# Optimization experiments

Hardware: AMD Instinct MI355X
Metric: run time of the kernel (lower is better)

## Reference

```python
import jax, jax.numpy as jnp
import numpy as np
from jax import lax

M, N, D = 4096, 4096, 256
SINKHORN_ITERATIONS = 100
SINKHORN_EPSILON = 0.1
DESC_SCALE = 0.05  # keep exp(S/eps) finite for random descriptors


def setup_inputs() -> dict:
    key = jax.random.key(0)
    k1, k2 = jax.random.split(key)
    d_M_q = jax.random.normal(k1, (M, D), dtype=jnp.float32) * DESC_SCALE
    d_N_r = jax.random.normal(k2, (N, D), dtype=jnp.float32) * DESC_SCALE
    z = jnp.float32(0.5)  # SuperGlue bin_score default
    return {"d_M_q": d_M_q, "d_N_r": d_N_r, "z": z}


def reference(d_M_q, d_N_r, z):
    m, n = d_M_q.shape[0], d_N_r.shape[0]
    # score matrix [M, N]
    S = jnp.einsum('md,nd->mn', d_M_q, d_N_r)
    # augment with dustbin row/col filled with z -> [M+1, N+1]
    dtype = d_M_q.dtype
    last_col = jnp.full((m, 1), z, dtype=dtype)
    last_row = jnp.full((1, n + 1), z, dtype=dtype)
    S_aug = jnp.concatenate([jnp.concatenate([S, last_col], axis=1), last_row], axis=0)
    K = jnp.exp(S_aug / SINKHORN_EPSILON)

    def step(K, _):
        K = K / K.sum(axis=1, keepdims=True)  # row normalize
        K = K / K.sum(axis=0, keepdims=True)  # col normalize
        return K, None

    K, _ = lax.scan(step, K, None, length=SINKHORN_ITERATIONS)
    P = K[:m, :n]
    return P, K
```

## Files before the change

### kernel.cpp

```cpp
#include <hip/hip_runtime.h>
#include <hip/hip_bf16.h>


#define MROWS 4096
#define NCOLS 4096
#define DDIM 256
#define MP1 4097
#define INV_EPS 10.0f
#define NBLK 256
#define XSLOT 4160
#define BAR_DW 160

typedef __attribute__((ext_vector_type(8))) short bf16x8;
typedef __attribute__((ext_vector_type(4))) float f32x4;
typedef __attribute__((ext_vector_type(2))) float f32x2;
typedef __attribute__((ext_vector_type(4))) unsigned short u16x4;

static __device__ __forceinline__ unsigned short f2bf(float f) {
  __hip_bfloat16 h = __float2bfloat16(f);
  union { __hip_bfloat16 h; unsigned short s; } c;
  c.h = h;
  return c.s;
}

static __device__ __forceinline__ void ld_strip(const float* ps, float4& xv) {
  asm volatile("global_load_dwordx4 %0, %1, off sc0\n\t"
               "s_waitcnt vmcnt(0)"
               : "=v"(xv) : "v"(ps) : "memory");
}
static __device__ __forceinline__ void ld_strip_dust(const float* ps, const float* pd,
                                                     float4& xv, float& xd) {
  asm volatile("global_load_dwordx4 %0, %2, off sc0\n\t"
               "global_load_dword %1, %3, off sc0\n\t"
               "s_waitcnt vmcnt(0)"
               : "=v"(xv), "=v"(xd)
               : "v"(ps), "v"(pd)
               : "memory");
}
static __device__ __forceinline__ void st_coherent(float* p, float x) {
  asm volatile("global_store_dword %0, %1, off sc0 sc1" :: "v"(p), "v"(x) : "memory");
}
static __device__ __forceinline__ unsigned ld_flagc(const unsigned* p) {
  unsigned r;
  asm volatile("global_load_dword %0, %1, off sc0 sc1\n\t"
               "s_waitcnt vmcnt(0)"
               : "=v"(r) : "v"(p) : "memory");
  return r;
}

template <int MODE>
__global__ __launch_bounds__(256) void mfma_gemm_kernel(
    const float* __restrict__ Q, const float* __restrict__ R,
    unsigned char* __restrict__ A8, unsigned char* __restrict__ T8,
    float* __restrict__ Kf, float* __restrict__ P,
    const float* __restrict__ u, const float* __restrict__ v)
{
  __shared__ unsigned short Qs[128][40];
  __shared__ unsigned short Rs[128][40];

  const int tid = threadIdx.x;
  const int lane = tid & 63;
  const int wid = tid >> 6;
  const int wy = wid >> 1;
  const int wx = wid & 1;
  const int rb = blockIdx.y * 128;
  const int cb = blockIdx.x * 128;
  const int lr = tid >> 3;
  const int lf = (tid & 7) * 4;

  f32x4 acc[4][4];
#pragma unroll
  for (int m = 0; m < 4; ++m)
#pragma unroll
    for (int n = 0; n < 4; ++n)
      acc[m][n] = (f32x4){0.f, 0.f, 0.f, 0.f};

  for (int k0 = 0; k0 < DDIM; k0 += 32) {
    float4 qv[4], rv[4];
#pragma unroll
    for (int i = 0; i < 4; ++i) {
      qv[i] = *reinterpret_cast<const float4*>(&Q[(size_t)(rb + lr + 32 * i) * DDIM + k0 + lf]);
      rv[i] = *reinterpret_cast<const float4*>(&R[(size_t)(cb + lr + 32 * i) * DDIM + k0 + lf]);
    }
    __syncthreads();
#pragma unroll
    for (int i = 0; i < 4; ++i) {
      u16x4 qs = {f2bf(qv[i].x), f2bf(qv[i].y), f2bf(qv[i].z), f2bf(qv[i].w)};
      u16x4 rs = {f2bf(rv[i].x), f2bf(rv[i].y), f2bf(rv[i].z), f2bf(rv[i].w)};
      *reinterpret_cast<u16x4*>(&Qs[lr + 32 * i][lf]) = qs;
      *reinterpret_cast<u16x4*>(&Rs[lr + 32 * i][lf]) = rs;
    }
    __syncthreads();

    const int ko = (lane >> 4) * 8;
    const int fr = lane & 15;
    bf16x8 af[4], bg[4];
#pragma unroll
    for (int m = 0; m < 4; ++m)
      af[m] = *reinterpret_cast<const bf16x8*>(&Qs[wy * 64 + m * 16 + fr][ko]);
#pragma unroll
    for (int n = 0; n < 4; ++n)
      bg[n] = *reinterpret_cast<const bf16x8*>(&Rs[wx * 64 + n * 16 + fr][ko]);
#pragma unroll
    for (int m = 0; m < 4; ++m)
#pragma unroll
      for (int n = 0; n < 4; ++n)
        acc[m][n] = __builtin_amdgcn_mfma_f32_16x16x32_bf16(af[m], bg[n], acc[m][n], 0, 0, 0);
  }

  const int r0 = (lane >> 4) * 4;
  const int fc = lane & 15;
#pragma unroll
  for (int m = 0; m < 4; ++m) {
    const int row0 = rb + wy * 64 + m * 16 + r0;
    float uu[4];
    if (MODE == 1) {
#pragma unroll
      for (int r = 0; r < 4; ++r) uu[r] = u[row0 + r];
    }
#pragma unroll
    for (int n = 0; n < 4; ++n) {
      const int col = cb + wx * 64 + n * 16 + fc;
      if (MODE == 0) {
        float kv[4];
#pragma unroll
        for (int r = 0; r < 4; ++r) kv[r] = __expf(acc[m][n][r] * INV_EPS);
        int packed = __builtin_amdgcn_cvt_pk_fp8_f32(kv[0], kv[1], 0, false);
        packed = __builtin_amdgcn_cvt_pk_fp8_f32(kv[2], kv[3], packed, true);
        *reinterpret_cast<unsigned int*>(&T8[(size_t)col * NCOLS + row0]) = (unsigned int)packed;
#pragma unroll
        for (int r = 0; r < 4; ++r)
          A8[(size_t)(row0 + r) * NCOLS + col] = (unsigned char)(((unsigned int)packed >> (8 * r)) & 0xffu);
      } else {
        const float vc = v[col];
#pragma unroll
        for (int r = 0; r < 4; ++r) {
          const float kv = __expf(acc[m][n][r] * INV_EPS);
          const float val = uu[r] * kv * vc;
          Kf[(size_t)(row0 + r) * MP1 + col] = val;
          P[(size_t)(row0 + r) * NCOLS + col] = val;
        }
      }
    }
  }
}

__global__ void init_sync_kernel(float* __restrict__ xbuf, unsigned* __restrict__ bar)
{
  const int i = blockIdx.x * 1024 + threadIdx.x;
  if (i < MP1) xbuf[i] = 1.0f;
  if (i < BAR_DW) bar[i] = 0u;
}

__global__ void edgeK_kernel(const float* __restrict__ zp, float* __restrict__ Kf,
                             const float* __restrict__ u, const float* __restrict__ v)
{
  const int i = blockIdx.x * 256 + threadIdx.x;
  if (i >= MP1) return;
  const float E = __expf(zp[0] * INV_EPS);
  Kf[(size_t)i * MP1 + NCOLS] = u[i] * E * v[NCOLS];
  Kf[(size_t)MROWS * MP1 + i] = u[MROWS] * E * v[i];
}

__global__ __launch_bounds__(1024) void sinkhorn_persist_kernel(
    const unsigned char* __restrict__ A8, const unsigned char* __restrict__ T8,
    float* __restrict__ xbuf, const float* __restrict__ zp,
    unsigned* __restrict__ bar)
{
  __shared__ unsigned char lA[16 * 4096];
  __shared__ unsigned char lT[16 * 4096];
  __shared__ float scratch[2][16][17];
  __shared__ float dscr[2][16];

  const int tid = threadIdx.x;
  const int b = blockIdx.x;
  const int lane = tid & 63;
  const int w = tid >> 6;
  const float E = __expf(zp[0] * INV_EPS);
  const int rev4 = ((lane & 1) << 3) | ((lane & 2) << 1) | ((lane & 4) >> 1) | ((lane & 8) >> 3);

  unsigned* cg  = bar + ((b & 7) << 4);
  unsigned* cm  = bar + 128;
  unsigned* gen = bar + 144;

  {
    const uint4* gA = reinterpret_cast<const uint4*>(A8 + (size_t)b * 16 * 4096);
    const uint4* gT = reinterpret_cast<const uint4*>(T8 + (size_t)b * 16 * 4096);
    uint4* sA = reinterpret_cast<uint4*>(lA);
    uint4* sT = reinterpret_cast<uint4*>(lT);
#pragma unroll
    for (int i = 0; i < 4; ++i) {
      sA[tid + 1024 * i] = gA[tid + 1024 * i];
      sT[tid + 1024 * i] = gT[tid + 1024 * i];
    }
  }
  __syncthreads();

  const int c0 = (w << 8) + (lane << 2);

  for (int g = 1; g <= 200; ++g) {
    const unsigned char* Kl = (g & 1) ? lA : lT;
    const float* xin = xbuf + (size_t)(g - 1) * XSLOT;
    float* xout = xbuf + (size_t)g * XSLOT;
    const unsigned need = (unsigned)(g - 1);
    const int sb = g & 1;

    if (tid == 0) {
      unsigned gv = ld_flagc(gen);
      while (gv < need) {
        __builtin_amdgcn_s_sleep(1);
        gv = ld_flagc(gen);
      }
    }
    __syncthreads();

    float4 xv; float xd = 0.f;
    if (w == 0) ld_strip_dust(xin + c0, xin + 4096, xv, xd);
    else        ld_strip(xin + c0, xv);

    float acc[16];
#pragma unroll
    for (int r = 0; r < 16; ++r) {
      const unsigned int aw = *reinterpret_cast<const unsigned int*>(Kl + r * 4096 + c0);
      const f32x2 lo = __builtin_amdgcn_cvt_pk_f32_fp8((int)aw, false);
      const f32x2 hi = __builtin_amdgcn_cvt_pk_f32_fp8((int)aw, true);
      acc[r] = lo.x * xv.x + lo.y * xv.y + hi.x * xv.z + hi.y * xv.w;
    }

    float r8[8], r4[4], r2[2], r1;
    {
      const bool f0 = (lane & 1) != 0;
#pragma unroll
      for (int k = 0; k < 8; ++k) {
        const float send = f0 ? acc[k] : acc[k + 8];
        const float keep = f0 ? acc[k + 8] : acc[k];
        r8[k] = keep + __shfl_xor(send, 1, 64);
      }
      const bool f1 = (lane & 2) != 0;
#pragma unroll
      for (int k = 0; k < 4; ++k) {
        const float send = f1 ? r8[k] : r8[k + 4];
        const float keep = f1 ? r8[k + 4] : r8[k];
        r4[k] = keep + __shfl_xor(send, 2, 64);
      }
      const bool f2 = (lane & 4) != 0;
#pragma unroll
      for (int k = 0; k < 2; ++k) {
        const float send = f2 ? r4[k] : r4[k + 2];
        const float keep = f2 ? r4[k + 2] : r4[k];
        r2[k] = keep + __shfl_xor(send, 4, 64);
      }
      const bool f3 = (lane & 8) != 0;
      {
        const float send = f3 ? r2[0] : r2[1];
        const float keep = f3 ? r2[1] : r2[0];
        r1 = keep + __shfl_xor(send, 8, 64);
      }
      r1 += __shfl_xor(r1, 16, 64);
      r1 += __shfl_xor(r1, 32, 64);
    }
    if (lane < 16) scratch[sb][rev4][w] = r1;

    if (b == 0) {
      float sv = xv.x + xv.y + xv.z + xv.w;
      sv += __shfl_xor(sv, 1, 64);  sv += __shfl_xor(sv, 2, 64);
      sv += __shfl_xor(sv, 4, 64);  sv += __shfl_xor(sv, 8, 64);
      sv += __shfl_xor(sv, 16, 64); sv += __shfl_xor(sv, 32, 64);
      if (lane == 0) dscr[sb][w] = sv;
    }
    __syncthreads();

    if (w == 0) {
      const int rr = lane >> 2, wq = (lane & 3) * 4;
      float s = scratch[sb][rr][wq] + scratch[sb][rr][wq + 1]
              + scratch[sb][rr][wq + 2] + scratch[sb][rr][wq + 3];
      s += __shfl_xor(s, 1, 64);
      s += __shfl_xor(s, 2, 64);
      if ((lane & 3) == 0)
        st_coherent(xout + (b << 4) + rr, 1.0f / (s + E * xd));
      if (b == 0) {
        float t = (lane < 16) ? dscr[sb][lane] : 0.f;
        t += __shfl_xor(t, 1, 64);  t += __shfl_xor(t, 2, 64);
        t += __shfl_xor(t, 4, 64);  t += __shfl_xor(t, 8, 64);
        t += __shfl_xor(t, 16, 64); t += __shfl_xor(t, 32, 64);
        if (lane == 0) st_coherent(xout + 4096, 1.0f / (E * (t + xd)));
      }
      asm volatile("s_waitcnt vmcnt(0)" ::: "memory");
      if (lane == 0) {
        const unsigned a = __hip_atomic_fetch_add(cg, 1u, __ATOMIC_RELAXED,
                                                  __HIP_MEMORY_SCOPE_AGENT);
        if (a == 32u * (unsigned)g - 1u) {
          const unsigned m = __hip_atomic_fetch_add(cm, 1u, __ATOMIC_RELAXED,
                                                    __HIP_MEMORY_SCOPE_AGENT);
          if (m == 8u * (unsigned)g - 1u)
            __hip_atomic_store(gen, (unsigned)g, __ATOMIC_RELAXED,
                               __HIP_MEMORY_SCOPE_AGENT);
        }
      }
    }
  }
}

extern "C" void kernel_launch(void* const* d_in, const int* in_sizes, int n_in,
                              void* d_out, int out_size, void* d_ws, size_t ws_size,
                              hipStream_t stream) {
  const float* Q = (const float*)d_in[0];
  const float* R = (const float*)d_in[1];
  const float* z = (const float*)d_in[2];

  float* P = (float*)d_out;
  float* Kf = P + (size_t)MROWS * NCOLS;

  unsigned char* A8 = (unsigned char*)d_ws;
  unsigned char* T8 = A8 + (size_t)MROWS * NCOLS;
  float* xbuf = (float*)(T8 + (size_t)MROWS * NCOLS);
  unsigned* bar = (unsigned*)(xbuf + (size_t)201 * XSLOT);

  const float* u_final = xbuf + (size_t)199 * XSLOT;
  const float* v_final = xbuf + (size_t)200 * XSLOT;

  mfma_gemm_kernel<0><<<dim3(32, 32), 256, 0, stream>>>(Q, R, A8, T8, nullptr, nullptr, nullptr, nullptr);
  init_sync_kernel<<<5, 1024, 0, stream>>>(xbuf, bar);
  sinkhorn_persist_kernel<<<NBLK, 1024, 0, stream>>>(A8, T8, xbuf, z, bar);
  mfma_gemm_kernel<1><<<dim3(32, 32), 256, 0, stream>>>(Q, R, nullptr, nullptr, Kf, P, u_final, v_final);
  edgeK_kernel<<<(MP1 + 255) / 256, 256, 0, stream>>>(z, Kf, u_final, v_final);
}
```

Before: 1.044 ms.

## Replace two-level grid barrier with per-group release flags and ring-buffered vectors

Drops the second-level atomic counter and the single generation flag. Each of the 8 group counters now publishes its own release flag, and a whole wavefront polls all 8 flags at once with __all, removing one serialized atomic hop from every barrier. The scaling-vector history shrinks from 201 slots to a 4-slot ring, and the vector loads now use sc0 sc1 to bypass caches so they stay coherent. The risks are an extra polling load per lane and that init_sync_kernel (not shown) must reset the new flag layout correctly.

```diff
diff --git a/kernel.cpp b/kernel.cpp
--- a/kernel.cpp
+++ b/kernel.cpp
@@ -24,14 +24,14 @@
 }
 
 static __device__ __forceinline__ void ld_strip(const float* ps, float4& xv) {
-  asm volatile("global_load_dwordx4 %0, %1, off sc0\n\t"
+  asm volatile("global_load_dwordx4 %0, %1, off sc0 sc1\n\t"
                "s_waitcnt vmcnt(0)"
                : "=v"(xv) : "v"(ps) : "memory");
 }
 static __device__ __forceinline__ void ld_strip_dust(const float* ps, const float* pd,
                                                      float4& xv, float& xd) {
-  asm volatile("global_load_dwordx4 %0, %2, off sc0\n\t"
-               "global_load_dword %1, %3, off sc0\n\t"
+  asm volatile("global_load_dwordx4 %0, %2, off sc0 sc1\n\t"
+               "global_load_dword %1, %3, off sc0 sc1\n\t"
                "s_waitcnt vmcnt(0)"
                : "=v"(xv), "=v"(xd)
                : "v"(ps), "v"(pd)
@@ -46,6 +46,9 @@
                "s_waitcnt vmcnt(0)"
                : "=v"(r) : "v"(p) : "memory");
   return r;
+}
+static __device__ __forceinline__ void st_flag(unsigned* p, unsigned x) {
+  asm volatile("global_store_dword %0, %1, off sc0 sc1" :: "v"(p), "v"(x) : "memory");
 }
 
 template <int MODE>
@@ -179,9 +182,8 @@
   const float E = __expf(zp[0] * INV_EPS);
   const int rev4 = ((lane & 1) << 3) | ((lane & 2) << 1) | ((lane & 4) >> 1) | ((lane & 8) >> 3);
 
-  unsigned* cg  = bar + ((b & 7) << 4);
-  unsigned* cm  = bar + 128;
-  unsigned* gen = bar + 144;
+  unsigned* cg = bar + ((b & 7) << 4);
+  unsigned* release = bar + 128;
 
   {
     const uint4* gA = reinterpret_cast<const uint4*>(A8 + (size_t)b * 16 * 4096);
@@ -200,16 +202,16 @@
 
   for (int g = 1; g <= 200; ++g) {
     const unsigned char* Kl = (g & 1) ? lA : lT;
-    const float* xin = xbuf + (size_t)(g - 1) * XSLOT;
-    float* xout = xbuf + (size_t)g * XSLOT;
+    const float* xin = xbuf + (size_t)((g - 1) & 3) * XSLOT;
+    float* xout = xbuf + (size_t)(g & 3) * XSLOT;
     const unsigned need = (unsigned)(g - 1);
     const int sb = g & 1;
 
-    if (tid == 0) {
-      unsigned gv = ld_flagc(gen);
-      while (gv < need) {
+    if (w == 0) {
+      unsigned fv = ld_flagc(release + (lane & 7));
+      while (!__all((int)(fv >= need))) {
         __builtin_amdgcn_s_sleep(1);
-        gv = ld_flagc(gen);
+        fv = ld_flagc(release + (lane & 7));
       }
     }
     __syncthreads();
@@ -289,13 +291,8 @@
       if (lane == 0) {
         const unsigned a = __hip_atomic_fetch_add(cg, 1u, __ATOMIC_RELAXED,
                                                   __HIP_MEMORY_SCOPE_AGENT);
-        if (a == 32u * (unsigned)g - 1u) {
-          const unsigned m = __hip_atomic_fetch_add(cm, 1u, __ATOMIC_RELAXED,
-                                                    __HIP_MEMORY_SCOPE_AGENT);
-          if (m == 8u * (unsigned)g - 1u)
-            __hip_atomic_store(gen, (unsigned)g, __ATOMIC_RELAXED,
-                               __HIP_MEMORY_SCOPE_AGENT);
-        }
+        if (a == 32u * (unsigned)g - 1u)
+          st_flag(release + (b & 7), (unsigned)g);
       }
     }
   }
@@ -314,10 +311,10 @@
   unsigned char* A8 = (unsigned char*)d_ws;
   unsigned char* T8 = A8 + (size_t)MROWS * NCOLS;
   float* xbuf = (float*)(T8 + (size_t)MROWS * NCOLS);
-  unsigned* bar = (unsigned*)(xbuf + (size_t)201 * XSLOT);
-
-  const float* u_final = xbuf + (size_t)199 * XSLOT;
-  const float* v_final = xbuf + (size_t)200 * XSLOT;
+  unsigned* bar = (unsigned*)(xbuf + (size_t)4 * XSLOT);
+
+  const float* u_final = xbuf + (size_t)3 * XSLOT;
+  const float* v_final = xbuf;
 
   mfma_gemm_kernel<0><<<dim3(32, 32), 256, 0, stream>>>(Q, R, A8, T8, nullptr, nullptr, nullptr, nullptr);
   init_sync_kernel<<<5, 1024, 0, stream>>>(xbuf, bar);
```

After: 924.3 us. 1.13x faster.
